# Optimization experiments

Measured on AMD Instinct MI355X. Metric: run time of the kernel, lower is better.

Reference implementation:

```python
import jax, jax.numpy as jnp
import numpy as np

B, N_IMFS, SEQ, FEAT = 64, 8, 128, 8
EPS = 1e-08


def setup_inputs() -> dict:
    key = jax.random.key(0)
    x = jax.random.normal(key, (B, N_IMFS, SEQ, FEAT), dtype=jnp.float32)
    return {"x": x}


def reference(x) -> jnp.ndarray:
    # x: [B, n_imfs, seq_len, feat]
    # torch.std uses Bessel's correction (ddof=1), reduction over seq axis
    std = jnp.std(x, axis=2, keepdims=True, ddof=1)            # [B, I, 1, F]
    scaled = jnp.where(std > 0, x / (std * 2), x)              # [B, I, S, F]
    scaled = jnp.clip(scaled, -1 + EPS, 1 - EPS)
    phi = jnp.arccos(scaled)                                   # [B, I, S, F]
    # summation method: gasf[i,j] = cos(phi_i + phi_j)
    gasf = jnp.cos(phi[:, :, :, None, :] + phi[:, :, None, :, :])  # [B, I, S, S, F]
    return gasf
```

## Files before the change

kernel.cpp:

```cpp
#include <hip/hip_runtime.h>


constexpr int SEQ  = 128;
constexpr int FEAT = 8;
constexpr int BI   = 64 * 8;
constexpr int CHUNKS = 4;
constexpr int ROWS_PER_CHUNK = SEQ / CHUNKS;

__global__ __launch_bounds__(256) void gasf_kernel(const float* __restrict__ x,
                                                   float* __restrict__ out) {
    __shared__ float a_s[SEQ * FEAT];
    __shared__ float c_s[SEQ * FEAT];
    __shared__ float inv_s[FEAT];

    const int tid   = threadIdx.x;
    const int pair  = blockIdx.x >> 2;
    const int chunk = blockIdx.x & 3;

    const float* xp = x + (size_t)pair * (SEQ * FEAT);

    reinterpret_cast<float4*>(a_s)[tid] = reinterpret_cast<const float4*>(xp)[tid];
    __syncthreads();

    if (tid < 64) {
        const int f   = tid >> 3;
        const int sub = tid & 7;
        float sum = 0.0f, sq = 0.0f;
#pragma unroll
        for (int k = 0; k < 16; ++k) {
            float v = a_s[(sub + 8 * k) * FEAT + f];
            sum += v;
            sq = fmaf(v, v, sq);
        }
#pragma unroll
        for (int d = 1; d < 8; d <<= 1) {
            sum += __shfl_xor(sum, d);
            sq  += __shfl_xor(sq, d);
        }
        const float mean = sum * (1.0f / SEQ);
        const float var  = fmaxf((sq - sum * mean) * (1.0f / (SEQ - 1)), 0.0f);
        const float sd   = sqrtf(var);
        inv_s[f] = (sd > 0.0f) ? (1.0f / (2.0f * sd)) : 1.0f;
    }
    __syncthreads();

    {
        float4 v = reinterpret_cast<const float4*>(a_s)[tid];
        const int f0 = (tid * 4) & 7;
        const float lo = -1.0f + 1e-8f;
        const float hi =  1.0f - 1e-8f;
        float vv[4] = {v.x, v.y, v.z, v.w};
        float a[4], c[4];
#pragma unroll
        for (int j = 0; j < 4; ++j) {
            float s = vv[j] * inv_s[f0 + j];
            s = fminf(fmaxf(s, lo), hi);
            a[j] = s;
            c[j] = sqrtf(fmaxf(fmaf(-s, s, 1.0f), 0.0f));
        }
        reinterpret_cast<float4*>(a_s)[tid] = make_float4(a[0], a[1], a[2], a[3]);
        reinterpret_cast<float4*>(c_s)[tid] = make_float4(c[0], c[1], c[2], c[3]);
    }
    __syncthreads();

    const int s2   = tid & 127;
    const int half = tid >> 7;
    const float4 a2l = *reinterpret_cast<const float4*>(a_s + s2 * FEAT);
    const float4 a2h = *reinterpret_cast<const float4*>(a_s + s2 * FEAT + 4);
    const float4 c2l = *reinterpret_cast<const float4*>(c_s + s2 * FEAT);
    const float4 c2h = *reinterpret_cast<const float4*>(c_s + s2 * FEAT + 4);

    float* outp = out + (size_t)pair * (SEQ * SEQ * FEAT) + (size_t)s2 * FEAT;
    const int s1_base = chunk * ROWS_PER_CHUNK + half;

#pragma unroll
    for (int k = 0; k < 16; ++k) {
        const int s1 = s1_base + 2 * k;
        const float* ap = a_s + s1 * FEAT;
        const float* cp = c_s + s1 * FEAT;
        const float4 a1l = *reinterpret_cast<const float4*>(ap);
        const float4 a1h = *reinterpret_cast<const float4*>(ap + 4);
        const float4 c1l = *reinterpret_cast<const float4*>(cp);
        const float4 c1h = *reinterpret_cast<const float4*>(cp + 4);

        float4 ol, oh;
        ol.x = fmaf(a1l.x, a2l.x, -(c1l.x * c2l.x));
        ol.y = fmaf(a1l.y, a2l.y, -(c1l.y * c2l.y));
        ol.z = fmaf(a1l.z, a2l.z, -(c1l.z * c2l.z));
        ol.w = fmaf(a1l.w, a2l.w, -(c1l.w * c2l.w));
        oh.x = fmaf(a1h.x, a2h.x, -(c1h.x * c2h.x));
        oh.y = fmaf(a1h.y, a2h.y, -(c1h.y * c2h.y));
        oh.z = fmaf(a1h.z, a2h.z, -(c1h.z * c2h.z));
        oh.w = fmaf(a1h.w, a2h.w, -(c1h.w * c2h.w));

        float* dst = outp + (size_t)s1 * (SEQ * FEAT);
        reinterpret_cast<float4*>(dst)[0] = ol;
        reinterpret_cast<float4*>(dst)[1] = oh;
    }
}

extern "C" void kernel_launch(void* const* d_in, const int* in_sizes, int n_in,
                              void* d_out, int out_size, void* d_ws, size_t ws_size,
                              hipStream_t stream) {
    const float* x = (const float*)d_in[0];
    float* out = (float*)d_out;
    gasf_kernel<<<dim3(BI * CHUNKS), dim3(256), 0, stream>>>(x, out);
}
```

Baseline: 257.1 us.

## Remap store loop to contiguous 16-byte-per-lane row writes with nontemporal stores

The output-writing loop is reorganized so each of the 256 threads owns one float4 column slice of a full output row. A wavefront now writes one contiguous region per iteration, where before each lane issued two float4 stores to separate halves of its 32-byte element, and it loops over all 32 rows of its chunk. Stores use __builtin_nontemporal_store to avoid polluting caches with the write-once 32MB output. This should coalesce writes better and cut the LDS reads per store, though the nontemporal hint could hurt write-combining on some paths.

```diff
diff --git a/kernel.cpp b/kernel.cpp
--- a/kernel.cpp
+++ b/kernel.cpp
@@ -5,7 +5,9 @@
 constexpr int FEAT = 8;
 constexpr int BI   = 64 * 8;
 constexpr int CHUNKS = 4;
-constexpr int ROWS_PER_CHUNK = SEQ / CHUNKS;
+constexpr int ROWS = SEQ / CHUNKS;
+
+typedef float v4f __attribute__((ext_vector_type(4)));
 
 __global__ __launch_bounds__(256) void gasf_kernel(const float* __restrict__ x,
                                                    float* __restrict__ out) {
@@ -19,7 +21,7 @@
 
     const float* xp = x + (size_t)pair * (SEQ * FEAT);
 
-    reinterpret_cast<float4*>(a_s)[tid] = reinterpret_cast<const float4*>(xp)[tid];
+    reinterpret_cast<v4f*>(a_s)[tid] = reinterpret_cast<const v4f*>(xp)[tid];
     __syncthreads();
 
     if (tid < 64) {
@@ -45,57 +47,46 @@
     __syncthreads();
 
     {
-        float4 v = reinterpret_cast<const float4*>(a_s)[tid];
+        v4f v = reinterpret_cast<const v4f*>(a_s)[tid];
         const int f0 = (tid * 4) & 7;
         const float lo = -1.0f + 1e-8f;
         const float hi =  1.0f - 1e-8f;
-        float vv[4] = {v.x, v.y, v.z, v.w};
-        float a[4], c[4];
+        v4f a, c;
 #pragma unroll
         for (int j = 0; j < 4; ++j) {
-            float s = vv[j] * inv_s[f0 + j];
+            float s = v[j] * inv_s[f0 + j];
             s = fminf(fmaxf(s, lo), hi);
             a[j] = s;
             c[j] = sqrtf(fmaxf(fmaf(-s, s, 1.0f), 0.0f));
         }
-        reinterpret_cast<float4*>(a_s)[tid] = make_float4(a[0], a[1], a[2], a[3]);
-        reinterpret_cast<float4*>(c_s)[tid] = make_float4(c[0], c[1], c[2], c[3]);
+        reinterpret_cast<v4f*>(a_s)[tid] = a;
+        reinterpret_cast<v4f*>(c_s)[tid] = c;
     }
     __syncthreads();
 
-    const int s2   = tid & 127;
-    const int half = tid >> 7;
-    const float4 a2l = *reinterpret_cast<const float4*>(a_s + s2 * FEAT);
-    const float4 a2h = *reinterpret_cast<const float4*>(a_s + s2 * FEAT + 4);
-    const float4 c2l = *reinterpret_cast<const float4*>(c_s + s2 * FEAT);
-    const float4 c2h = *reinterpret_cast<const float4*>(c_s + s2 * FEAT + 4);
+    const int col_off = tid * 4;
+    const v4f a2 = *reinterpret_cast<const v4f*>(a_s + col_off);
+    const v4f c2 = *reinterpret_cast<const v4f*>(c_s + col_off);
+    const int fh4 = (tid & 1) * 4;
 
-    float* outp = out + (size_t)pair * (SEQ * SEQ * FEAT) + (size_t)s2 * FEAT;
-    const int s1_base = chunk * ROWS_PER_CHUNK + half;
+    const int s1_0 = chunk * ROWS;
+    float* rowp = out + (size_t)pair * (SEQ * SEQ * FEAT)
+                      + (size_t)s1_0 * (SEQ * FEAT) + col_off;
 
 #pragma unroll
-    for (int k = 0; k < 16; ++k) {
-        const int s1 = s1_base + 2 * k;
-        const float* ap = a_s + s1 * FEAT;
-        const float* cp = c_s + s1 * FEAT;
-        const float4 a1l = *reinterpret_cast<const float4*>(ap);
-        const float4 a1h = *reinterpret_cast<const float4*>(ap + 4);
-        const float4 c1l = *reinterpret_cast<const float4*>(cp);
-        const float4 c1h = *reinterpret_cast<const float4*>(cp + 4);
+    for (int k = 0; k < ROWS; ++k) {
+        const int s1 = s1_0 + k;
+        const v4f a1 = *reinterpret_cast<const v4f*>(a_s + s1 * FEAT + fh4);
+        const v4f c1 = *reinterpret_cast<const v4f*>(c_s + s1 * FEAT + fh4);
 
-        float4 ol, oh;
-        ol.x = fmaf(a1l.x, a2l.x, -(c1l.x * c2l.x));
-        ol.y = fmaf(a1l.y, a2l.y, -(c1l.y * c2l.y));
-        ol.z = fmaf(a1l.z, a2l.z, -(c1l.z * c2l.z));
-        ol.w = fmaf(a1l.w, a2l.w, -(c1l.w * c2l.w));
-        oh.x = fmaf(a1h.x, a2h.x, -(c1h.x * c2h.x));
-        oh.y = fmaf(a1h.y, a2h.y, -(c1h.y * c2h.y));
-        oh.z = fmaf(a1h.z, a2h.z, -(c1h.z * c2h.z));
-        oh.w = fmaf(a1h.w, a2h.w, -(c1h.w * c2h.w));
+        v4f o;
+        o.x = fmaf(a1.x, a2.x, -(c1.x * c2.x));
+        o.y = fmaf(a1.y, a2.y, -(c1.y * c2.y));
+        o.z = fmaf(a1.z, a2.z, -(c1.z * c2.z));
+        o.w = fmaf(a1.w, a2.w, -(c1.w * c2.w));
 
-        float* dst = outp + (size_t)s1 * (SEQ * FEAT);
-        reinterpret_cast<float4*>(dst)[0] = ol;
-        reinterpret_cast<float4*>(dst)[1] = oh;
+        __builtin_nontemporal_store(o, reinterpret_cast<v4f*>(rowp));
+        rowp += SEQ * FEAT;
     }
 }
 
```

Measured after the change: 264.0 us. +2.7%, slower.
